# Optimization experiments

Hardware: AMD Instinct MI355X
Metric: run time of the kernel (lower is better)

## Reference

```python
import jax, jax.numpy as jnp
import numpy as np

N, L, C, H = 8, 2048, 512, 512
C_HALF = max(C // 2, 1)


def setup_inputs() -> dict:
    key = jax.random.key(0)
    ks = jax.random.split(key, 11)
    s = 0.02
    return {
        "x": jax.random.normal(ks[0], (N, L, C), dtype=jnp.float32),
        "theta_w": jax.random.normal(ks[1], (C, H), dtype=jnp.float32) * s,
        "theta_b": jax.random.normal(ks[2], (H,), dtype=jnp.float32) * s,
        "phi_w": jax.random.normal(ks[3], (C, H), dtype=jnp.float32) * s,
        "phi_b": jax.random.normal(ks[4], (H,), dtype=jnp.float32) * s,
        "psi_w": jax.random.normal(ks[5], (C, H), dtype=jnp.float32) * s,
        "psi_b": jax.random.normal(ks[6], (H,), dtype=jnp.float32) * s,
        "r1_w": jax.random.normal(ks[7], (H, C_HALF), dtype=jnp.float32) * s,
        "r1_b": jax.random.normal(ks[8], (C_HALF,), dtype=jnp.float32) * s,
        "r2_w": jax.random.normal(ks[9], (C_HALF, C), dtype=jnp.float32) * s,
        "r2_b": jax.random.normal(ks[10], (C,), dtype=jnp.float32) * s,
    }


def reference(x, theta_w, theta_b, phi_w, phi_b, psi_w, psi_b, r1_w, r1_b, r2_w, r2_b):
    # projections: [n, L, h]
    x_t = x @ theta_w + theta_b
    x_ph = x @ phi_w + phi_b
    x_psi = x @ psi_w + psi_b
    # unscaled attention: phi @ theta^T -> [n, L, L], softmax over last dim
    attn = jax.nn.softmax(jnp.einsum("nlh,nmh->nlm", x_ph, x_t), axis=2)
    x_add = jnp.einsum("nlm,nmh->nlh", attn, x_psi)
    # recover MLP with LeakyReLU(0.2) then Tanh, residual add
    h1 = jax.nn.leaky_relu(x_add @ r1_w + r1_b, negative_slope=0.2)
    h2 = jnp.tanh(h1 @ r2_w + r2_b)
    return x + h2
```

## Files before the change

### kernel.cpp

```cpp
#include <hip/hip_runtime.h>
#include <hip/hip_bf16.h>

typedef float f32x4 __attribute__((ext_vector_type(4)));
typedef int   v8i   __attribute__((ext_vector_type(8)));
typedef __attribute__((address_space(3))) unsigned int       lds_uint;
typedef __attribute__((address_space(1))) const unsigned int glb_uint;

__device__ __forceinline__ float tanh_fast(float x) {
    float e = __expf(-2.0f * fabsf(x));
    float r = (1.0f - e) / (1.0f + e);
    return copysignf(r, x);
}
__device__ __forceinline__ unsigned char f2fp8(float v) {
    return (unsigned char)(__builtin_amdgcn_cvt_pk_fp8_f32(v, 0.0f, 0, false) & 0xff);
}
__device__ __forceinline__ unsigned short f2h(float v) {
    _Float16 h = (_Float16)v;
    unsigned short u;
    __builtin_memcpy(&u, &h, 2);
    return u;
}
__device__ __forceinline__ float h2f(unsigned short u) {
    _Float16 h;
    __builtin_memcpy(&h, &u, 2);
    return (float)h;
}

__global__ __launch_bounds__(256) void prep(
    const float* __restrict__ x,
    const float* __restrict__ theta_w, const float* __restrict__ phi_w,
    const float* __restrict__ psi_w,   const float* __restrict__ r1_w,
    const float* __restrict__ r2_w,
    const float* __restrict__ theta_b, const float* __restrict__ phi_b,
    const float* __restrict__ psi_b,
    unsigned char* __restrict__ xb8, unsigned char* __restrict__ wCat8T,
    unsigned char* __restrict__ r1T8, unsigned char* __restrict__ r2T8,
    float* __restrict__ bCat) {
    const int b = blockIdx.x, t = threadIdx.x;
    if (b < 8192) {
        long i = ((long)b * 256 + t) * 4;
        float4 f = *(const float4*)(x + i);
        int w = __builtin_amdgcn_cvt_pk_fp8_f32(f.x, f.y, 0, false);
        w = __builtin_amdgcn_cvt_pk_fp8_f32(f.z, f.w, w, true);
        *(unsigned int*)(xb8 + i) = (unsigned int)w;
    } else if (b < 11264) {
        const int sel = (b - 8192) >> 10;
        const int idx = ((b - 8192) & 1023) * 256 + t;
        const float* w = sel == 0 ? theta_w : (sel == 1 ? phi_w : psi_w);
        const int r = idx >> 9, c = idx & 511;
        wCat8T[(long)(sel * 512 + c) * 512 + r] = f2fp8(w[idx] * 16.0f);
    } else if (b < 11776) {
        const int idx = (b - 11264) * 256 + t;
        const int r = idx >> 8, c = idx & 255;
        r1T8[(long)c * 512 + r] = f2fp8(r1_w[idx] * 16.0f);
    } else if (b < 12288) {
        const int idx = (b - 11776) * 256 + t;
        const int r = idx >> 9, c = idx & 511;
        r2T8[(long)c * 256 + r] = f2fp8(r2_w[idx] * 16.0f);
    } else {
        const int i = (b - 12288) * 256 + t;
        if (i < 1536)
            bCat[i] = i < 512 ? theta_b[i] : (i < 1024 ? phi_b[i - 512] : psi_b[i - 1024]);
    }
}

__global__ __launch_bounds__(256) void softmax_fp8(unsigned short* __restrict__ S) {
    const size_t row = (size_t)blockIdx.y * 2048 + blockIdx.x;
    unsigned short* p = S + row * 2048;
    const int t = threadIdx.x;
    uint4 raw = *(uint4*)(p + t * 8);
    unsigned int w[4] = {raw.x, raw.y, raw.z, raw.w};
    float v[8];
#pragma unroll
    for (int i = 0; i < 4; ++i) {
        v[2 * i]     = h2f((unsigned short)(w[i] & 0xffffu));
        v[2 * i + 1] = h2f((unsigned short)(w[i] >> 16));
    }
    float mx = v[0];
#pragma unroll
    for (int i = 1; i < 8; ++i) mx = fmaxf(mx, v[i]);
#pragma unroll
    for (int off = 32; off > 0; off >>= 1) mx = fmaxf(mx, __shfl_xor(mx, off));
    __shared__ float red[8];
    const int wave = t >> 6, lane = t & 63;
    if (lane == 0) red[wave] = mx;
    __syncthreads();
    mx = fmaxf(fmaxf(red[0], red[1]), fmaxf(red[2], red[3]));
    float s = 0.0f;
#pragma unroll
    for (int i = 0; i < 8; ++i) { v[i] = __expf(v[i] - mx); s += v[i]; }
#pragma unroll
    for (int off = 32; off > 0; off >>= 1) s += __shfl_xor(s, off);
    if (lane == 0) red[4 + wave] = s;
    __syncthreads();
    s = red[4] + red[5] + red[6] + red[7];
    const float inv = 1.0f / s;
    int o0 = __builtin_amdgcn_cvt_pk_fp8_f32(v[0] * inv, v[1] * inv, 0, false);
    o0 = __builtin_amdgcn_cvt_pk_fp8_f32(v[2] * inv, v[3] * inv, o0, true);
    int o1 = __builtin_amdgcn_cvt_pk_fp8_f32(v[4] * inv, v[5] * inv, 0, false);
    o1 = __builtin_amdgcn_cvt_pk_fp8_f32(v[6] * inv, v[7] * inv, o1, true);
    uint2 ov; ov.x = (unsigned int)o0; ov.y = (unsigned int)o1;
    *(uint2*)((unsigned char*)p + t * 8) = ov;
}

template <int MODE>
__global__ __launch_bounds__(256) void gemm_fp8(
    const unsigned char* __restrict__ A,
    const unsigned char* __restrict__ Bt,
    const float* __restrict__ bias,
    const float* __restrict__ resid,
    unsigned short* __restrict__ outH,
    unsigned char* __restrict__ out8,
    unsigned char* __restrict__ out8b,
    unsigned char* __restrict__ outV,
    float* __restrict__ outF,
    int K, int ldaB, int ldbB, int ldc, long sA, long sB, long sC) {
    __shared__ unsigned char As[128 * 128];
    __shared__ unsigned char Bs[128 * 128];

    const int tid  = threadIdx.x;
    const int lane = tid & 63, wave = tid >> 6;
    const int m16  = lane & 15, quad = lane >> 4;
    const int wm   = (wave >> 1) << 6, wn = (wave & 1) << 6;
    const int m0   = blockIdx.x << 7, n0 = blockIdx.y << 7;

    const int srow = lane >> 3;
    const int uswz = (lane & 7) ^ srow;

    const unsigned char* Abase = A  + (long)blockIdx.z * sA + (long)m0 * ldaB;
    const unsigned char* Bbase = Bt + (long)blockIdx.z * sB + (long)n0 * ldbB;
    const int stR = (wave << 5) + srow;
    const long gA0 = (long)stR * ldaB + (uswz << 4);
    const long gB0 = (long)stR * ldbB + (uswz << 4);

    const int s8  = m16 & 7;
    const int P   = quad ^ (s8 >> 1);
    const int cLo = (P << 1) + (s8 & 1);
    const int offLo = cLo << 4;
    const int offHi = (cLo ^ 1) << 4;

    f32x4 acc[4][4] = {};

    union F8 { v8i v; int4 q[2]; };

    for (int k0 = 0; k0 < K; k0 += 128) {
        __syncthreads();
#pragma unroll
        for (int i = 0; i < 4; ++i) {
            const unsigned char* gp = Abase + gA0 + (long)(i << 3) * ldaB + k0;
            unsigned char* lp = &As[(((wave << 5) + (i << 3)) << 7)];
            __builtin_amdgcn_global_load_lds((glb_uint*)gp, (lds_uint*)lp, 16, 0, 0);
        }
#pragma unroll
        for (int i = 0; i < 4; ++i) {
            const unsigned char* gp = Bbase + gB0 + (long)(i << 3) * ldbB + k0;
            unsigned char* lp = &Bs[(((wave << 5) + (i << 3)) << 7)];
            __builtin_amdgcn_global_load_lds((glb_uint*)gp, (lds_uint*)lp, 16, 0, 0);
        }
        __syncthreads();
        F8 af[4], bg[4];
#pragma unroll
        for (int f = 0; f < 4; ++f) {
            const int m = wm + (f << 4) + m16;
            const int n = wn + (f << 4) + m16;
            af[f].q[0] = *(const int4*)&As[(m << 7) + offLo];
            af[f].q[1] = *(const int4*)&As[(m << 7) + offHi];
            bg[f].q[0] = *(const int4*)&Bs[(n << 7) + offLo];
            bg[f].q[1] = *(const int4*)&Bs[(n << 7) + offHi];
        }
#pragma unroll
        for (int fi = 0; fi < 4; ++fi)
#pragma unroll
            for (int fj = 0; fj < 4; ++fj)
                acc[fi][fj] = __builtin_amdgcn_mfma_scale_f32_16x16x128_f8f6f4(
                    af[fi].v, bg[fj].v, acc[fi][fj],
                    0, 0,
                    0, 127,
                    0, 127);
    }

    const long zC = (long)blockIdx.z * sC;

    if (MODE == 0) {
        const int sel = n0 >> 9;
        if (sel < 2) {
            unsigned char* dst = sel == 0 ? out8 : out8b;
#pragma unroll
            for (int fj = 0; fj < 4; ++fj) {
                const int col = n0 + wn + (fj << 4) + m16;
                const int cb  = col & 511;
                const float bv = bias[col];
#pragma unroll
                for (int fi = 0; fi < 4; ++fi)
#pragma unroll
                    for (int r = 0; r < 4; ++r) {
                        const int row = m0 + wm + (fi << 4) + (quad << 2) + r;
                        dst[(long)row * 512 + cb] = f2fp8(acc[fi][fj][r] * 0.0625f + bv);
                    }
            }
        } else {
            const int z = m0 >> 11, l0 = (m0 & 2047) + wm + (quad << 2);
#pragma unroll
            for (int fj = 0; fj < 4; ++fj) {
                const int col = n0 + wn + (fj << 4) + m16;
                const int h   = col & 511;
                const float bv = bias[col];
#pragma unroll
                for (int fi = 0; fi < 4; ++fi) {
                    int w = __builtin_amdgcn_cvt_pk_fp8_f32(
                        acc[fi][fj][0] * 0.0625f + bv, acc[fi][fj][1] * 0.0625f + bv, 0, false);
                    w = __builtin_amdgcn_cvt_pk_fp8_f32(
                        acc[fi][fj][2] * 0.0625f + bv, acc[fi][fj][3] * 0.0625f + bv, w, true);
                    *(unsigned int*)(outV + ((long)z * 512 + h) * 2048 + l0 + (fi << 4)) =
                        (unsigned int)w;
                }
            }
        }
    } else {
#pragma unroll
        for (int fj = 0; fj < 4; ++fj) {
            const int col = n0 + wn + (fj << 4) + m16;
            float bv = 0.0f;
            if (MODE >= 3) bv = bias[col];
#pragma unroll
            for (int fi = 0; fi < 4; ++fi)
#pragma unroll
                for (int r = 0; r < 4; ++r) {
                    const int row = m0 + wm + (fi << 4) + (quad << 2) + r;
                    float v = acc[fi][fj][r];
                    if (MODE == 1) {
                        outH[zC + (long)row * ldc + col] = f2h(v);
                    } else if (MODE == 2) {
                        out8[zC + (long)row * 512 + col] = f2fp8(v);
                    } else if (MODE == 3) {
                        v = v * 0.0625f + bv;
                        v = v > 0.0f ? v : 0.2f * v;
                        out8[(long)row * 256 + col] = f2fp8(v);
                    } else {
                        v = v * 0.0625f + bv;
                        const long idx = (long)row * ldc + col;
                        outF[idx] = tanh_fast(v) + resid[idx];
                    }
                }
        }
    }
}

extern "C" void kernel_launch(void* const* d_in, const int* in_sizes, int n_in,
                              void* d_out, int out_size, void* d_ws, size_t ws_size,
                              hipStream_t stream) {
    const float* x       = (const float*)d_in[0];
    const float* theta_w = (const float*)d_in[1];
    const float* theta_b = (const float*)d_in[2];
    const float* phi_w   = (const float*)d_in[3];
    const float* phi_b   = (const float*)d_in[4];
    const float* psi_w   = (const float*)d_in[5];
    const float* psi_b   = (const float*)d_in[6];
    const float* r1_w    = (const float*)d_in[7];
    const float* r1_b    = (const float*)d_in[8];
    const float* r2_w    = (const float*)d_in[9];
    const float* r2_b    = (const float*)d_in[10];
    float* out = (float*)d_out;

    constexpr int  N = 8, L = 2048, C = 512, H = 512, CH = 256;
    constexpr long NL = (long)N * L;

    char* p = (char*)d_ws;
    auto alloc = [&](size_t bytes) { void* q = (void*)p; p += bytes; return q; };
    unsigned char*  xb8    = (unsigned char*)alloc(NL * C);
    unsigned char*  TH8    = (unsigned char*)alloc(NL * H);
    unsigned char*  PH8    = (unsigned char*)alloc(NL * H);
    unsigned char*  VT8    = (unsigned char*)alloc((long)N * H * L);
    unsigned char*  xadd8  = (unsigned char*)alloc(NL * H);
    unsigned char*  h18    = (unsigned char*)alloc(NL * CH);
    unsigned char*  wCat8T = (unsigned char*)alloc((long)1536 * 512);
    unsigned char*  r1T8   = (unsigned char*)alloc((long)H * CH);
    unsigned char*  r2T8   = (unsigned char*)alloc((long)CH * C);
    float*          bCat   = (float*)alloc(1536 * 4 + 256);
    unsigned short* S      = (unsigned short*)alloc((long)N * L * L * 2);

    prep<<<12294, 256, 0, stream>>>(x, theta_w, phi_w, psi_w, r1_w, r2_w,
                                    theta_b, phi_b, psi_b, xb8, wCat8T, r1T8, r2T8, bCat);

    gemm_fp8<0><<<dim3(NL / 128, 1536 / 128, 1), 256, 0, stream>>>(
        xb8, wCat8T, bCat, nullptr, nullptr, TH8, PH8, VT8, nullptr,
        C, C, C, 0, 0, 0, 0);

    gemm_fp8<1><<<dim3(L / 128, L / 128, N), 256, 0, stream>>>(
        PH8, TH8, nullptr, nullptr, S, nullptr, nullptr, nullptr, nullptr,
        H, H, H, L, (long)L * H, (long)L * H, (long)L * L);

    softmax_fp8<<<dim3(L, N), 256, 0, stream>>>(S);

    gemm_fp8<2><<<dim3(L / 128, H / 128, N), 256, 0, stream>>>(
        (const unsigned char*)S, VT8, nullptr, nullptr, nullptr, xadd8, nullptr, nullptr, nullptr,
        L, 2 * L, L, H, (long)L * 2 * L, (long)H * L, (long)L * H);

    gemm_fp8<3><<<dim3(NL / 128, CH / 128, 1), 256, 0, stream>>>(
        xadd8, r1T8, r1_b, nullptr, nullptr, h18, nullptr, nullptr, nullptr,
        H, H, H, CH, 0, 0, 0);

    gemm_fp8<4><<<dim3(NL / 128, C / 128, 1), 256, 0, stream>>>(
        h18, r2T8, r2_b, x, nullptr, nullptr, nullptr, nullptr, out,
        CH, CH, CH, C, 0, 0, 0);
}
```

Baseline: 226.2 us.

## Double-buffer LDS tiles in fp8 GEMM to overlap global loads with MFMA

Doubles the shared-memory A/B tiles and issues the next k-tile's global-to-LDS loads before computing the current one. Manual vmcnt/lgkmcnt waits and raw barriers replace the two __syncthreads per iteration, so memory latency can be hidden behind MFMA work. LDS use doubles to 64KB per block, which may reduce occupancy. Correctness now relies on hand-placed waitcnt counts.

```diff
diff --git a/kernel.cpp b/kernel.cpp
--- a/kernel.cpp
+++ b/kernel.cpp
@@ -115,8 +115,8 @@
     unsigned char* __restrict__ outV,
     float* __restrict__ outF,
     int K, int ldaB, int ldbB, int ldc, long sA, long sB, long sC) {
-    __shared__ unsigned char As[128 * 128];
-    __shared__ unsigned char Bs[128 * 128];
+    __shared__ unsigned char As[2][128 * 128];
+    __shared__ unsigned char Bs[2][128 * 128];
 
     const int tid  = threadIdx.x;
     const int lane = tid & 63, wave = tid >> 6;
@@ -143,30 +143,43 @@
 
     union F8 { v8i v; int4 q[2]; };
 
+    auto STAGE = [&](int buf, int kk) {
+#pragma unroll
+        for (int i = 0; i < 4; ++i) {
+            const unsigned char* gp = Abase + gA0 + (long)(i << 3) * ldaB + kk;
+            unsigned char* lp = &As[buf][((wave << 5) + (i << 3)) << 7];
+            __builtin_amdgcn_global_load_lds((glb_uint*)gp, (lds_uint*)lp, 16, 0, 0);
+        }
+#pragma unroll
+        for (int i = 0; i < 4; ++i) {
+            const unsigned char* gp = Bbase + gB0 + (long)(i << 3) * ldbB + kk;
+            unsigned char* lp = &Bs[buf][((wave << 5) + (i << 3)) << 7];
+            __builtin_amdgcn_global_load_lds((glb_uint*)gp, (lds_uint*)lp, 16, 0, 0);
+        }
+    };
+
+    STAGE(0, 0);
+    int cur = 0;
     for (int k0 = 0; k0 < K; k0 += 128) {
-        __syncthreads();
-#pragma unroll
-        for (int i = 0; i < 4; ++i) {
-            const unsigned char* gp = Abase + gA0 + (long)(i << 3) * ldaB + k0;
-            unsigned char* lp = &As[(((wave << 5) + (i << 3)) << 7)];
-            __builtin_amdgcn_global_load_lds((glb_uint*)gp, (lds_uint*)lp, 16, 0, 0);
-        }
-#pragma unroll
-        for (int i = 0; i < 4; ++i) {
-            const unsigned char* gp = Bbase + gB0 + (long)(i << 3) * ldbB + k0;
-            unsigned char* lp = &Bs[(((wave << 5) + (i << 3)) << 7)];
-            __builtin_amdgcn_global_load_lds((glb_uint*)gp, (lds_uint*)lp, 16, 0, 0);
-        }
-        __syncthreads();
+        if (k0 + 128 < K) {
+            STAGE(cur ^ 1, k0 + 128);
+            asm volatile("s_waitcnt vmcnt(8)" ::: "memory");
+        } else {
+            asm volatile("s_waitcnt vmcnt(0)" ::: "memory");
+        }
+        asm volatile("s_barrier" ::: "memory");
+
+        const unsigned char* Ab = As[cur];
+        const unsigned char* Bb = Bs[cur];
         F8 af[4], bg[4];
 #pragma unroll
         for (int f = 0; f < 4; ++f) {
             const int m = wm + (f << 4) + m16;
             const int n = wn + (f << 4) + m16;
-            af[f].q[0] = *(const int4*)&As[(m << 7) + offLo];
-            af[f].q[1] = *(const int4*)&As[(m << 7) + offHi];
-            bg[f].q[0] = *(const int4*)&Bs[(n << 7) + offLo];
-            bg[f].q[1] = *(const int4*)&Bs[(n << 7) + offHi];
+            af[f].q[0] = *(const int4*)&Ab[(m << 7) + offLo];
+            af[f].q[1] = *(const int4*)&Ab[(m << 7) + offHi];
+            bg[f].q[0] = *(const int4*)&Bb[(n << 7) + offLo];
+            bg[f].q[1] = *(const int4*)&Bb[(n << 7) + offHi];
         }
 #pragma unroll
         for (int fi = 0; fi < 4; ++fi)
@@ -177,6 +190,10 @@
                     0, 0,
                     0, 127,
                     0, 127);
+
+        asm volatile("s_waitcnt lgkmcnt(0)" ::: "memory");
+        asm volatile("s_barrier" ::: "memory");
+        cur ^= 1;
     }
 
     const long zC = (long)blockIdx.z * sC;
```

Result: no change. 223.6 us (-1.2%).
